# Performance work log

Measured on AMD Instinct MI355X. Metric: run time of the kernel, lower is better.

The kernel has to match this reference:

```python
import jax, jax.numpy as jnp
import numpy as np

B, S, D, H, K = 2, 2048, 1024, 16, 64


def setup_inputs() -> dict:
    key = jax.random.key(0)
    k1, k2, k3 = jax.random.split(key, 3)
    x = jax.random.normal(k1, (B, S, D), dtype=jnp.float32)
    # causal mask: 1 where query can attend to key (key_pos <= pos)
    mask = jnp.tril(jnp.ones((S, S), dtype=jnp.float32))
    W_qkv = jax.random.normal(k2, (D, 3, H, K), dtype=jnp.float32) * 0.02
    b_qkv = jnp.zeros((3, H, K), dtype=jnp.float32)
    W_proj = jax.random.normal(k3, (H, K, D), dtype=jnp.float32) * 0.02
    b_proj = jnp.zeros((D,), dtype=jnp.float32)
    return {"x": x, "mask": mask, "W_qkv": W_qkv, "b_qkv": b_qkv,
            "W_proj": W_proj, "b_proj": b_proj, "layer_idx": 0}


def reference(x, mask, W_qkv, b_qkv, W_proj, b_proj, layer_idx):
    # c_attn: [B,S,D] @ [D,3,H,K] -> [B,S,3,H,K]
    qkv = jnp.einsum('bsd,dthk->bsthk', x, W_qkv) + b_qkv
    q, k, v = qkv[:, :, 0], qkv[:, :, 1], qkv[:, :, 2]  # each [B,S,H,K]
    scale = jax.lax.rsqrt(float(K))  # scale_attn_by_inverse_layer_idx=False
    q = q * scale
    # attn scores over key_size: [B,H,S(pos),S(key_pos)]
    scores = jnp.einsum('bshk,bthk->bhst', q, k)
    scores = scores + (1.0 - mask) * -1e9
    weights = jax.nn.softmax(scores, axis=-1).astype(x.dtype)
    # attn_pdrop = 0.0 -> dropout is identity
    attn_out = jnp.einsum('bhst,bthk->bshk', weights, v)  # [B,S,H,K]
    out = jnp.einsum('bshk,hkd->bsd', attn_out, W_proj) + b_proj
    return out
```

## Files before the change

### kernel.cpp

```cpp
#include <hip/hip_runtime.h>

typedef __bf16 bf16x8 __attribute__((ext_vector_type(8)));
typedef float f32x4 __attribute__((ext_vector_type(4)));
typedef float f32x16 __attribute__((ext_vector_type(16)));
typedef unsigned short u16x8 __attribute__((ext_vector_type(8)));

constexpr int S_LEN = 2048;
constexpr int QKV1  = 2 * 16 * 2048 * 64;

__device__ inline unsigned short f2bf(float f) {
    __bf16 h = (__bf16)f;
    return __builtin_bit_cast(unsigned short, h);
}

__device__ inline void gll16(const void* g, void* l) {
    __builtin_amdgcn_global_load_lds(
        (const __attribute__((address_space(1))) unsigned int*)g,
        (__attribute__((address_space(3))) unsigned int*)l,
        16, 0, 0);
}

__global__ __launch_bounds__(256) void cvt_f32_bf16(
    const float* __restrict__ src, unsigned short* __restrict__ dst, int n4)
{
    int i = blockIdx.x * 256 + threadIdx.x;
    if (i >= n4) return;
    float4 v = ((const float4*)src)[i];
    ushort4 u;
    u.x = f2bf(v.x); u.y = f2bf(v.y); u.z = f2bf(v.z); u.w = f2bf(v.w);
    ((ushort4*)dst)[i] = u;
}

__global__ __launch_bounds__(256) void transpose_cvt(
    const float* __restrict__ src, unsigned short* __restrict__ dst, int R, int C)
{
    __shared__ float t[32][33];
    const int c0 = blockIdx.x * 32, r0 = blockIdx.y * 32;
    const int tx = threadIdx.x, ty = threadIdx.y;
    #pragma unroll
    for (int i = 0; i < 4; ++i)
        t[ty * 4 + i][tx] = src[(size_t)(r0 + ty * 4 + i) * C + c0 + tx];
    __syncthreads();
    #pragma unroll
    for (int i = 0; i < 4; ++i)
        dst[(size_t)(c0 + ty * 4 + i) * R + r0 + tx] = f2bf(t[tx][ty * 4 + i]);
}

template<int EPI>
__global__ __launch_bounds__(256) void gemm128(
    const unsigned short* __restrict__ A,
    const unsigned short* __restrict__ Bt,
    const float* __restrict__ bias,
    void* __restrict__ outp, int M, int N, int K)
{
    __shared__ unsigned short As[128 * 64];
    __shared__ unsigned short Bs[128 * 64];
    const int tid = threadIdx.x, lane = tid & 63, wid = tid >> 6;
    const int q = lane & 15, g = lane >> 4;
    const int wr = wid >> 1, wc = wid & 1;

    const int nbx = N >> 7;
    const int cpx = gridDim.x >> 3;
    const int bid = blockIdx.x;
    const int swz = (bid & 7) * cpx + (bid >> 3);
    const int m0 = (swz / nbx) * 128, n0 = (swz % nbx) * 128;

    const int lrow = lane >> 3, lcol = (lane & 7) * 8;

    f32x4 acc[4][4];
    #pragma unroll
    for (int i = 0; i < 4; ++i)
        #pragma unroll
        for (int j = 0; j < 4; ++j) acc[i][j] = (f32x4){0.f, 0.f, 0.f, 0.f};

    for (int k0 = 0; k0 < K; k0 += 64) {
        #pragma unroll
        for (int i = 0; i < 4; ++i) {
            int c = wid * 4 + i;
            int row = c * 8 + lrow;
            gll16(&A [(size_t)(m0 + row) * K + k0 + lcol], &As[c * 512]);
            gll16(&Bt[(size_t)(n0 + row) * K + k0 + lcol], &Bs[c * 512]);
        }
        __syncthreads();
        #pragma unroll
        for (int h = 0; h < 2; ++h) {
            bf16x8 a[4], b[4];
            #pragma unroll
            for (int mi = 0; mi < 4; ++mi)
                a[mi] = *(const bf16x8*)&As[(wr * 64 + mi * 16 + q) * 64 + h * 32 + g * 8];
            #pragma unroll
            for (int ni = 0; ni < 4; ++ni)
                b[ni] = *(const bf16x8*)&Bs[(wc * 64 + ni * 16 + q) * 64 + h * 32 + g * 8];
            #pragma unroll
            for (int mi = 0; mi < 4; ++mi)
                #pragma unroll
                for (int ni = 0; ni < 4; ++ni)
                    acc[mi][ni] = __builtin_amdgcn_mfma_f32_16x16x32_bf16(a[mi], b[ni], acc[mi][ni], 0, 0, 0);
        }
        __syncthreads();
    }

    #pragma unroll
    for (int mi = 0; mi < 4; ++mi)
        #pragma unroll
        for (int ni = 0; ni < 4; ++ni)
            #pragma unroll
            for (int r = 0; r < 4; ++r) {
                int m = m0 + wr * 64 + mi * 16 + g * 4 + r;
                int n = n0 + wc * 64 + ni * 16 + q;
                float v = acc[mi][ni][r] + bias[n];
                if (EPI == 0) {
                    int t = n >> 10, rem = n & 1023;
                    if (t == 0) v *= 0.125f;
                    int h2 = rem >> 6, kk = rem & 63;
                    int bb = m >> 11, s = m & 2047;
                    ((unsigned short*)outp)[(size_t)t * QKV1 +
                        ((size_t)(bb * 16 + h2) * 2048 + s) * 64 + kk] = f2bf(v);
                } else {
                    ((float*)outp)[(size_t)m * N + n] = v;
                }
            }
}

__global__ __launch_bounds__(256) void attn_fwd(
    const unsigned short* __restrict__ qkv, unsigned short* __restrict__ aout)
{
    __shared__ unsigned short Ks[2][64][72];
    __shared__ unsigned short Vs[2][64][72];
    __shared__ float cLds[4][32];
    const int tid = threadIdx.x, lane = tid & 63, wid = tid >> 6;
    const int hi = lane >> 5, lq = lane & 31;
    const int bh = blockIdx.x, pr = blockIdx.y;
    const unsigned short* Qg = qkv + (size_t)bh * S_LEN * 64;
    const unsigned short* Kg = qkv + (size_t)QKV1 + (size_t)bh * S_LEN * 64;
    const unsigned short* Vg = qkv + 2 * (size_t)QKV1 + (size_t)bh * S_LEN * 64;

    const int srow = tid >> 2, sc = tid & 3;
    u16x8 kr0, kr1, vr0, vr1;
    auto stage_load = [&](int j0) {
        kr0 = *(const u16x8*)&Kg[(size_t)(j0 + srow) * 64 + sc * 16];
        kr1 = *(const u16x8*)&Kg[(size_t)(j0 + srow) * 64 + sc * 16 + 8];
        vr0 = *(const u16x8*)&Vg[(size_t)(j0 + srow) * 64 + sc * 16];
        vr1 = *(const u16x8*)&Vg[(size_t)(j0 + srow) * 64 + sc * 16 + 8];
    };
    auto stage_write = [&](int b) {
        *(u16x8*)&Ks[b][srow][sc * 16]     = kr0;
        *(u16x8*)&Ks[b][srow][sc * 16 + 8] = kr1;
        #pragma unroll
        for (int e = 0; e < 8; ++e) {
            Vs[b][sc * 16 + e][srow]     = vr0[e];
            Vs[b][sc * 16 + 8 + e][srow] = vr1[e];
        }
    };

    const int bb = bh >> 4, h = bh & 15;

    for (int ph = 0; ph < 2; ++ph) {
        const int t = ph ? (15 - pr) : pr;
        const int NJ = 2 * t + 2;
        const int qbase = t * 128 + wid * 32;
        const int qg = qbase + lq;

        bf16x8 qf[4];
        #pragma unroll
        for (int kc = 0; kc < 4; ++kc)
            qf[kc] = *(const bf16x8*)&Qg[(size_t)qg * 64 + kc * 16 + hi * 8];

        f32x16 o0, o1;
        #pragma unroll
        for (int j = 0; j < 16; ++j) { o0[j] = 0.f; o1[j] = 0.f; }
        float m = -1e30f, lr = 0.f;

        stage_load(0);
        __syncthreads();
        stage_write(0);
        int cur = 0;

        for (int jb = 0; jb < NJ; ++jb) {
            const int j0 = jb * 64;
            if (jb + 1 < NJ) stage_load(j0 + 64);
            __syncthreads();

            if (j0 <= qbase + 31) {
                f32x16 s0, s1;
                #pragma unroll
                for (int j = 0; j < 16; ++j) { s0[j] = 0.f; s1[j] = 0.f; }
                #pragma unroll
                for (int kc = 0; kc < 4; ++kc) {
                    bf16x8 k0 = *(const bf16x8*)&Ks[cur][lq][kc * 16 + hi * 8];
                    bf16x8 k1 = *(const bf16x8*)&Ks[cur][32 + lq][kc * 16 + hi * 8];
                    s0 = __builtin_amdgcn_mfma_f32_32x32x16_bf16(k0, qf[kc], s0, 0, 0, 0);
                    s1 = __builtin_amdgcn_mfma_f32_32x32x16_bf16(k1, qf[kc], s1, 0, 0, 0);
                }
                if (j0 + 63 > qbase) {
                    #pragma unroll
                    for (int r = 0; r < 16; ++r) {
                        int kv0 = j0 + (r & 3) + 8 * (r >> 2) + 4 * hi;
                        if (kv0 > qg)      s0[r] = -1e30f;
                        if (kv0 + 32 > qg) s1[r] = -1e30f;
                    }
                }
                float tm[16];
                #pragma unroll
                for (int j = 0; j < 16; ++j) tm[j] = fmaxf(s0[j], s1[j]);
                #pragma unroll
                for (int w = 8; w > 0; w >>= 1)
                    #pragma unroll
                    for (int j = 0; j < w; ++j) tm[j] = fmaxf(tm[j], tm[j + w]);
                float pm = fmaxf(tm[0], __shfl_xor(tm[0], 32));
                if (!__all(pm <= m + 8.0f)) {
                    float mn = fmaxf(m, pm);
                    float corr = __expf(m - mn);
                    m = mn; lr *= corr;
                    if (lane < 32) cLds[wid][lq] = corr;
                    #pragma unroll
                    for (int r = 0; r < 16; ++r) {
                        float cq = cLds[wid][(r & 3) + 8 * (r >> 2) + 4 * hi];
                        o0[r] *= cq; o1[r] *= cq;
                    }
                }
                float p0[16], p1[16], ts[16];
                #pragma unroll
                for (int j = 0; j < 16; ++j) {
                    p0[j] = __expf(s0[j] - m);
                    p1[j] = __expf(s1[j] - m);
                    ts[j] = p0[j] + p1[j];
                }
                #pragma unroll
                for (int w = 8; w > 0; w >>= 1)
                    #pragma unroll
                    for (int j = 0; j < w; ++j) ts[j] += ts[j + w];
                lr += ts[0] + __shfl_xor(ts[0], 32);
                int w0[8], w1[8];
                #pragma unroll
                for (int j = 0; j < 8; ++j) {
                    asm("v_cvt_pk_bf16_f32 %0, %1, %2" : "=v"(w0[j]) : "v"(p0[2 * j]), "v"(p0[2 * j + 1]));
                    asm("v_cvt_pk_bf16_f32 %0, %1, %2" : "=v"(w1[j]) : "v"(p1[2 * j]), "v"(p1[2 * j + 1]));
                }
                bf16x8 pa[4];
                auto mkfrag = [&](const int* w, int base) -> bf16x8 {
                    int x0 = __shfl_xor(w[base + 0], 32);
                    int x1 = __shfl_xor(w[base + 1], 32);
                    int x2 = __shfl_xor(w[base + 2], 32);
                    int x3 = __shfl_xor(w[base + 3], 32);
                    int4 f;
                    f.x = hi ? x2          : w[base + 0];
                    f.y = hi ? x3          : w[base + 1];
                    f.z = hi ? w[base + 2] : x0;
                    f.w = hi ? w[base + 3] : x1;
                    return __builtin_bit_cast(bf16x8, f);
                };
                pa[0] = mkfrag(w0, 0);
                pa[1] = mkfrag(w0, 4);
                pa[2] = mkfrag(w1, 0);
                pa[3] = mkfrag(w1, 4);
                #pragma unroll
                for (int kc = 0; kc < 4; ++kc) {
                    bf16x8 v0 = *(const bf16x8*)&Vs[cur][lq][kc * 16 + hi * 8];
                    bf16x8 v1 = *(const bf16x8*)&Vs[cur][32 + lq][kc * 16 + hi * 8];
                    o0 = __builtin_amdgcn_mfma_f32_32x32x16_bf16(pa[kc], v0, o0, 0, 0, 0);
                    o1 = __builtin_amdgcn_mfma_f32_32x32x16_bf16(pa[kc], v1, o1, 0, 0, 0);
                }
            }
            if (jb + 1 < NJ) stage_write(cur ^ 1);
            cur ^= 1;
        }

        float inv = 1.0f / lr;
        if (lane < 32) cLds[wid][lq] = inv;
        #pragma unroll
        for (int r = 0; r < 16; ++r) {
            float iq = cLds[wid][(r & 3) + 8 * (r >> 2) + 4 * hi];
            int srow_g = qbase + (r & 3) + 8 * (r >> 2) + 4 * hi;
            size_t rowoff = (size_t)(bb * 2048 + srow_g) * 1024 + h * 64;
            aout[rowoff + lq]      = f2bf(o0[r] * iq);
            aout[rowoff + 32 + lq] = f2bf(o1[r] * iq);
        }
        __syncthreads();
    }
}

extern "C" void kernel_launch(void* const* d_in, const int* in_sizes, int n_in,
                              void* d_out, int out_size, void* d_ws, size_t ws_size,
                              hipStream_t stream) {
    const float* x     = (const float*)d_in[0];
    const float* Wqkv  = (const float*)d_in[2];
    const float* bqkv  = (const float*)d_in[3];
    const float* Wproj = (const float*)d_in[4];
    const float* bproj = (const float*)d_in[5];

    unsigned short* qkvb  = (unsigned short*)d_ws;
    unsigned short* aoutb = qkvb + 3 * (size_t)QKV1;
    unsigned short* Wt   = aoutb;
    unsigned short* Wt2  = qkvb;
    unsigned short* Xbf  = (unsigned short*)d_out;

    cvt_f32_bf16<<<4096, 256, 0, stream>>>(x, Xbf, 4096 * 1024 / 4);
    transpose_cvt<<<dim3(96, 32), dim3(32, 8), 0, stream>>>(Wqkv, Wt, 1024, 3072);
    gemm128<0><<<768, 256, 0, stream>>>(Xbf, Wt, bqkv, qkvb, 4096, 3072, 1024);
    attn_fwd<<<dim3(32, 8), 256, 0, stream>>>(qkvb, aoutb);
    transpose_cvt<<<dim3(32, 32), dim3(32, 8), 0, stream>>>(Wproj, Wt2, 1024, 1024);
    gemm128<1><<<256, 256, 0, stream>>>(aoutb, Wt2, bproj, d_out, 4096, 1024, 1024);
}
```

Before: 150.0 us.

## Split attention into 64-row query blocks with 2 waves, drop pair scheduling

Each attention block now handles one 64-row query tile with two waves (128 threads) instead of a 128-row tile with four waves processing a paired short/long tile. The grid grows from 256 to 1024 blocks, launched longest-first. The per-wave skip of fully masked key blocks is gone because every key block now overlaps the tile. The goal is more blocks in flight on the CUs and less idle time from waves that had nothing to do in the pair scheme. The cost is that each staged K/V tile is reused by half as many query rows, and each thread performs more global loads per stage.

Result: slower. 166.9 us (+11.3%).

```diff
diff --git a/kernel.cpp b/kernel.cpp
--- a/kernel.cpp
+++ b/kernel.cpp
@@ -122,161 +122,156 @@
             }
 }
 
-__global__ __launch_bounds__(256) void attn_fwd(
+__global__ __launch_bounds__(128) void attn_fwd(
     const unsigned short* __restrict__ qkv, unsigned short* __restrict__ aout)
 {
     __shared__ unsigned short Ks[2][64][72];
     __shared__ unsigned short Vs[2][64][72];
-    __shared__ float cLds[4][32];
+    __shared__ float cLds[2][32];
     const int tid = threadIdx.x, lane = tid & 63, wid = tid >> 6;
     const int hi = lane >> 5, lq = lane & 31;
-    const int bh = blockIdx.x, pr = blockIdx.y;
+    const int bh = blockIdx.x;
+    const int t  = 31 - (int)blockIdx.y;
+    const int NJ = t + 1;
     const unsigned short* Qg = qkv + (size_t)bh * S_LEN * 64;
     const unsigned short* Kg = qkv + (size_t)QKV1 + (size_t)bh * S_LEN * 64;
     const unsigned short* Vg = qkv + 2 * (size_t)QKV1 + (size_t)bh * S_LEN * 64;
 
-    const int srow = tid >> 2, sc = tid & 3;
-    u16x8 kr0, kr1, vr0, vr1;
+    const int srr = tid >> 3, scc = (tid & 7) * 8;
+    u16x8 kr[4], vr[4];
     auto stage_load = [&](int j0) {
-        kr0 = *(const u16x8*)&Kg[(size_t)(j0 + srow) * 64 + sc * 16];
-        kr1 = *(const u16x8*)&Kg[(size_t)(j0 + srow) * 64 + sc * 16 + 8];
-        vr0 = *(const u16x8*)&Vg[(size_t)(j0 + srow) * 64 + sc * 16];
-        vr1 = *(const u16x8*)&Vg[(size_t)(j0 + srow) * 64 + sc * 16 + 8];
+        #pragma unroll
+        for (int p = 0; p < 4; ++p) {
+            kr[p] = *(const u16x8*)&Kg[(size_t)(j0 + srr + p * 16) * 64 + scc];
+            vr[p] = *(const u16x8*)&Vg[(size_t)(j0 + srr + p * 16) * 64 + scc];
+        }
     };
     auto stage_write = [&](int b) {
-        *(u16x8*)&Ks[b][srow][sc * 16]     = kr0;
-        *(u16x8*)&Ks[b][srow][sc * 16 + 8] = kr1;
-        #pragma unroll
-        for (int e = 0; e < 8; ++e) {
-            Vs[b][sc * 16 + e][srow]     = vr0[e];
-            Vs[b][sc * 16 + 8 + e][srow] = vr1[e];
+        #pragma unroll
+        for (int p = 0; p < 4; ++p) {
+            *(u16x8*)&Ks[b][srr + p * 16][scc] = kr[p];
+            #pragma unroll
+            for (int e = 0; e < 8; ++e)
+                Vs[b][scc + e][srr + p * 16] = vr[p][e];
         }
     };
 
     const int bb = bh >> 4, h = bh & 15;
-
-    for (int ph = 0; ph < 2; ++ph) {
-        const int t = ph ? (15 - pr) : pr;
-        const int NJ = 2 * t + 2;
-        const int qbase = t * 128 + wid * 32;
-        const int qg = qbase + lq;
-
-        bf16x8 qf[4];
-        #pragma unroll
-        for (int kc = 0; kc < 4; ++kc)
-            qf[kc] = *(const bf16x8*)&Qg[(size_t)qg * 64 + kc * 16 + hi * 8];
-
-        f32x16 o0, o1;
-        #pragma unroll
-        for (int j = 0; j < 16; ++j) { o0[j] = 0.f; o1[j] = 0.f; }
-        float m = -1e30f, lr = 0.f;
-
-        stage_load(0);
+    const int qbase = t * 64 + wid * 32;
+    const int qg = qbase + lq;
+
+    bf16x8 qf[4];
+    #pragma unroll
+    for (int kc = 0; kc < 4; ++kc)
+        qf[kc] = *(const bf16x8*)&Qg[(size_t)qg * 64 + kc * 16 + hi * 8];
+
+    f32x16 o0, o1;
+    #pragma unroll
+    for (int j = 0; j < 16; ++j) { o0[j] = 0.f; o1[j] = 0.f; }
+    float m = -1e30f, lr = 0.f;
+
+    stage_load(0);
+    stage_write(0);
+    int cur = 0;
+
+    for (int jb = 0; jb < NJ; ++jb) {
+        const int j0 = jb * 64;
+        if (jb + 1 < NJ) stage_load(j0 + 64);
         __syncthreads();
-        stage_write(0);
-        int cur = 0;
-
-        for (int jb = 0; jb < NJ; ++jb) {
-            const int j0 = jb * 64;
-            if (jb + 1 < NJ) stage_load(j0 + 64);
-            __syncthreads();
-
-            if (j0 <= qbase + 31) {
-                f32x16 s0, s1;
-                #pragma unroll
-                for (int j = 0; j < 16; ++j) { s0[j] = 0.f; s1[j] = 0.f; }
-                #pragma unroll
-                for (int kc = 0; kc < 4; ++kc) {
-                    bf16x8 k0 = *(const bf16x8*)&Ks[cur][lq][kc * 16 + hi * 8];
-                    bf16x8 k1 = *(const bf16x8*)&Ks[cur][32 + lq][kc * 16 + hi * 8];
-                    s0 = __builtin_amdgcn_mfma_f32_32x32x16_bf16(k0, qf[kc], s0, 0, 0, 0);
-                    s1 = __builtin_amdgcn_mfma_f32_32x32x16_bf16(k1, qf[kc], s1, 0, 0, 0);
-                }
-                if (j0 + 63 > qbase) {
-                    #pragma unroll
-                    for (int r = 0; r < 16; ++r) {
-                        int kv0 = j0 + (r & 3) + 8 * (r >> 2) + 4 * hi;
-                        if (kv0 > qg)      s0[r] = -1e30f;
-                        if (kv0 + 32 > qg) s1[r] = -1e30f;
-                    }
-                }
-                float tm[16];
-                #pragma unroll
-                for (int j = 0; j < 16; ++j) tm[j] = fmaxf(s0[j], s1[j]);
-                #pragma unroll
-                for (int w = 8; w > 0; w >>= 1)
-                    #pragma unroll
-                    for (int j = 0; j < w; ++j) tm[j] = fmaxf(tm[j], tm[j + w]);
-                float pm = fmaxf(tm[0], __shfl_xor(tm[0], 32));
-                if (!__all(pm <= m + 8.0f)) {
-                    float mn = fmaxf(m, pm);
-                    float corr = __expf(m - mn);
-                    m = mn; lr *= corr;
-                    if (lane < 32) cLds[wid][lq] = corr;
-                    #pragma unroll
-                    for (int r = 0; r < 16; ++r) {
-                        float cq = cLds[wid][(r & 3) + 8 * (r >> 2) + 4 * hi];
-                        o0[r] *= cq; o1[r] *= cq;
-                    }
-                }
-                float p0[16], p1[16], ts[16];
-                #pragma unroll
-                for (int j = 0; j < 16; ++j) {
-                    p0[j] = __expf(s0[j] - m);
-                    p1[j] = __expf(s1[j] - m);
-                    ts[j] = p0[j] + p1[j];
-                }
-                #pragma unroll
-                for (int w = 8; w > 0; w >>= 1)
-                    #pragma unroll
-                    for (int j = 0; j < w; ++j) ts[j] += ts[j + w];
-                lr += ts[0] + __shfl_xor(ts[0], 32);
-                int w0[8], w1[8];
-                #pragma unroll
-                for (int j = 0; j < 8; ++j) {
-                    asm("v_cvt_pk_bf16_f32 %0, %1, %2" : "=v"(w0[j]) : "v"(p0[2 * j]), "v"(p0[2 * j + 1]));
-                    asm("v_cvt_pk_bf16_f32 %0, %1, %2" : "=v"(w1[j]) : "v"(p1[2 * j]), "v"(p1[2 * j + 1]));
-                }
-                bf16x8 pa[4];
-                auto mkfrag = [&](const int* w, int base) -> bf16x8 {
-                    int x0 = __shfl_xor(w[base + 0], 32);
-                    int x1 = __shfl_xor(w[base + 1], 32);
-                    int x2 = __shfl_xor(w[base + 2], 32);
-                    int x3 = __shfl_xor(w[base + 3], 32);
-                    int4 f;
-                    f.x = hi ? x2          : w[base + 0];
-                    f.y = hi ? x3          : w[base + 1];
-                    f.z = hi ? w[base + 2] : x0;
-                    f.w = hi ? w[base + 3] : x1;
-                    return __builtin_bit_cast(bf16x8, f);
-                };
-                pa[0] = mkfrag(w0, 0);
-                pa[1] = mkfrag(w0, 4);
-                pa[2] = mkfrag(w1, 0);
-                pa[3] = mkfrag(w1, 4);
-                #pragma unroll
-                for (int kc = 0; kc < 4; ++kc) {
-                    bf16x8 v0 = *(const bf16x8*)&Vs[cur][lq][kc * 16 + hi * 8];
-                    bf16x8 v1 = *(const bf16x8*)&Vs[cur][32 + lq][kc * 16 + hi * 8];
-                    o0 = __builtin_amdgcn_mfma_f32_32x32x16_bf16(pa[kc], v0, o0, 0, 0, 0);
-                    o1 = __builtin_amdgcn_mfma_f32_32x32x16_bf16(pa[kc], v1, o1, 0, 0, 0);
-                }
+
+        f32x16 s0, s1;
+        #pragma unroll
+        for (int j = 0; j < 16; ++j) { s0[j] = 0.f; s1[j] = 0.f; }
+        #pragma unroll
+        for (int kc = 0; kc < 4; ++kc) {
+            bf16x8 k0 = *(const bf16x8*)&Ks[cur][lq][kc * 16 + hi * 8];
+            bf16x8 k1 = *(const bf16x8*)&Ks[cur][32 + lq][kc * 16 + hi * 8];
+            s0 = __builtin_amdgcn_mfma_f32_32x32x16_bf16(k0, qf[kc], s0, 0, 0, 0);
+            s1 = __builtin_amdgcn_mfma_f32_32x32x16_bf16(k1, qf[kc], s1, 0, 0, 0);
+        }
+        if (j0 + 63 > qbase) {
+            #pragma unroll
+            for (int r = 0; r < 16; ++r) {
+                int kv0 = j0 + (r & 3) + 8 * (r >> 2) + 4 * hi;
+                if (kv0 > qg)      s0[r] = -1e30f;
+                if (kv0 + 32 > qg) s1[r] = -1e30f;
             }
-            if (jb + 1 < NJ) stage_write(cur ^ 1);
-            cur ^= 1;
-        }
-
-        float inv = 1.0f / lr;
-        if (lane < 32) cLds[wid][lq] = inv;
-        #pragma unroll
-        for (int r = 0; r < 16; ++r) {
-            float iq = cLds[wid][(r & 3) + 8 * (r >> 2) + 4 * hi];
-            int srow_g = qbase + (r & 3) + 8 * (r >> 2) + 4 * hi;
-            size_t rowoff = (size_t)(bb * 2048 + srow_g) * 1024 + h * 64;
-            aout[rowoff + lq]      = f2bf(o0[r] * iq);
-            aout[rowoff + 32 + lq] = f2bf(o1[r] * iq);
-        }
-        __syncthreads();
+        }
+        float tm[16];
+        #pragma unroll
+        for (int j = 0; j < 16; ++j) tm[j] = fmaxf(s0[j], s1[j]);
+        #pragma unroll
+        for (int w = 8; w > 0; w >>= 1)
+            #pragma unroll
+            for (int j = 0; j < w; ++j) tm[j] = fmaxf(tm[j], tm[j + w]);
+        float pm = fmaxf(tm[0], __shfl_xor(tm[0], 32));
+        if (!__all(pm <= m + 8.0f)) {
+            float mn = fmaxf(m, pm);
+            float corr = __expf(m - mn);
+            m = mn; lr *= corr;
+            if (lane < 32) cLds[wid][lq] = corr;
+            #pragma unroll
+            for (int r = 0; r < 16; ++r) {
+                float cq = cLds[wid][(r & 3) + 8 * (r >> 2) + 4 * hi];
+                o0[r] *= cq; o1[r] *= cq;
+            }
+        }
+        float p0[16], p1[16], ts[16];
+        #pragma unroll
+        for (int j = 0; j < 16; ++j) {
+            p0[j] = __expf(s0[j] - m);
+            p1[j] = __expf(s1[j] - m);
+            ts[j] = p0[j] + p1[j];
+        }
+        #pragma unroll
+        for (int w = 8; w > 0; w >>= 1)
+            #pragma unroll
+            for (int j = 0; j < w; ++j) ts[j] += ts[j + w];
+        lr += ts[0] + __shfl_xor(ts[0], 32);
+        int w0[8], w1[8];
+        #pragma unroll
+        for (int j = 0; j < 8; ++j) {
+            asm("v_cvt_pk_bf16_f32 %0, %1, %2" : "=v"(w0[j]) : "v"(p0[2 * j]), "v"(p0[2 * j + 1]));
+            asm("v_cvt_pk_bf16_f32 %0, %1, %2" : "=v"(w1[j]) : "v"(p1[2 * j]), "v"(p1[2 * j + 1]));
+        }
+        bf16x8 pa[4];
+        auto mkfrag = [&](const int* w, int base) -> bf16x8 {
+            int x0 = __shfl_xor(w[base + 0], 32);
+            int x1 = __shfl_xor(w[base + 1], 32);
+            int x2 = __shfl_xor(w[base + 2], 32);
+            int x3 = __shfl_xor(w[base + 3], 32);
+            int4 f;
+            f.x = hi ? x2          : w[base + 0];
+            f.y = hi ? x3          : w[base + 1];
+            f.z = hi ? w[base + 2] : x0;
+            f.w = hi ? w[base + 3] : x1;
+            return __builtin_bit_cast(bf16x8, f);
+        };
+        pa[0] = mkfrag(w0, 0);
+        pa[1] = mkfrag(w0, 4);
+        pa[2] = mkfrag(w1, 0);
+        pa[3] = mkfrag(w1, 4);
+        #pragma unroll
+        for (int kc = 0; kc < 4; ++kc) {
+            bf16x8 v0 = *(const bf16x8*)&Vs[cur][lq][kc * 16 + hi * 8];
+            bf16x8 v1 = *(const bf16x8*)&Vs[cur][32 + lq][kc * 16 + hi * 8];
+            o0 = __builtin_amdgcn_mfma_f32_32x32x16_bf16(pa[kc], v0, o0, 0, 0, 0);
+            o1 = __builtin_amdgcn_mfma_f32_32x32x16_bf16(pa[kc], v1, o1, 0, 0, 0);
+        }
+
+        if (jb + 1 < NJ) stage_write(cur ^ 1);
+        cur ^= 1;
+    }
+
+    float inv = 1.0f / lr;
+    if (lane < 32) cLds[wid][lq] = inv;
+    #pragma unroll
+    for (int r = 0; r < 16; ++r) {
+        float iq = cLds[wid][(r & 3) + 8 * (r >> 2) + 4 * hi];
+        int srow_g = qbase + (r & 3) + 8 * (r >> 2) + 4 * hi;
+        size_t rowoff = (size_t)(bb * 2048 + srow_g) * 1024 + h * 64;
+        aout[rowoff + lq]      = f2bf(o0[r] * iq);
+        aout[rowoff + 32 + lq] = f2bf(o1[r] * iq);
     }
 }
 
@@ -298,7 +293,7 @@
     cvt_f32_bf16<<<4096, 256, 0, stream>>>(x, Xbf, 4096 * 1024 / 4);
     transpose_cvt<<<dim3(96, 32), dim3(32, 8), 0, stream>>>(Wqkv, Wt, 1024, 3072);
     gemm128<0><<<768, 256, 0, stream>>>(Xbf, Wt, bqkv, qkvb, 4096, 3072, 1024);
-    attn_fwd<<<dim3(32, 8), 256, 0, stream>>>(qkvb, aoutb);
+    attn_fwd<<<dim3(32, 32), 128, 0, stream>>>(qkvb, aoutb);
     transpose_cvt<<<dim3(32, 32), dim3(32, 8), 0, stream>>>(Wproj, Wt2, 1024, 1024);
     gemm128<1><<<256, 256, 0, stream>>>(aoutb, Wt2, bproj, d_out, 4096, 1024, 1024);
 }
```
